# Performance work log

Hardware: AMD Instinct MI355X
Metric: run time of the kernel (lower is better)

Reference implementation:

```python
import jax, jax.numpy as jnp
import numpy as np

B, LQ, LK = 4, 256, 512
DQ, DK, DV = 512, 512, 512
H = 256
NEG = -1e6


def setup_inputs() -> dict:
    key = jax.random.key(0)
    ks = jax.random.split(key, 7)
    queries = jax.random.normal(ks[0], (B, LQ, DQ), dtype=jnp.float32)
    keys = jax.random.normal(ks[1], (B, LK, DK), dtype=jnp.float32)
    values = jax.random.normal(ks[2], (B, LK, DV), dtype=jnp.float32)
    valid_lens = jax.random.randint(ks[3], (B,), 1, LK + 1).astype(jnp.int32)
    # learned params (Linear without bias): store as (in, out) so x @ W matches torch x @ W.T
    Wq = jax.random.normal(ks[4], (DQ, H), dtype=jnp.float32) * (1.0 / np.sqrt(DQ))
    Wk = jax.random.normal(ks[5], (DK, H), dtype=jnp.float32) * (1.0 / np.sqrt(DK))
    wv = jax.random.normal(ks[6], (H,), dtype=jnp.float32) * (1.0 / np.sqrt(H))
    return {"queries": queries, "keys": keys, "values": values,
            "valid_lens": valid_lens, "Wq": Wq, "Wk": Wk, "wv": wv}


def reference(queries, keys, values, valid_lens, Wq, Wk, wv):
    q = jnp.einsum('bqd,dh->bqh', queries, Wq)          # (B,Lq,H)
    k = jnp.einsum('bkd,dh->bkh', keys, Wk)             # (B,Lk,H)
    feats = jnp.tanh(q[:, :, None, :] + k[:, None, :, :])  # (B,Lq,Lk,H)
    scores = jnp.einsum('bqkh,h->bqk', feats, wv)        # (B,Lq,Lk)
    mask = jnp.arange(LK)[None, None, :] < valid_lens[:, None, None]  # (B,1,Lk)
    attn = jax.nn.softmax(jnp.where(mask, scores, NEG), axis=-1)
    return jnp.einsum('bqk,bkv->bqv', attn, values)      # (B,Lq,Dv)
```

## Files before the change

kernel.cpp:

```cpp
#include <hip/hip_runtime.h>
#include <hip/hip_fp16.h>

#define B_   4
#define LQ_  256
#define LK_  512
#define DIN_ 512
#define H_   256
#define DV_  512

#define L2E 1.4426950408889634f

__global__ __launch_bounds__(256) void proj_partial_kernel(
    const float* __restrict__ Q, const float* __restrict__ K,
    const float* __restrict__ Wq, const float* __restrict__ Wk,
    const int* __restrict__ valid_lens,
    float* __restrict__ qpart, float* __restrict__ ekTpart) {
  __shared__ float xs[64][68];
  __shared__ float ws[64][132];

  const int blk = blockIdx.x;
  const bool isQ = blk < 128;
  int b, row0, h0, ds;
  if (isQ) {
    ds = blk & 3; h0 = ((blk >> 2) & 1) * 128;
    const int rt = blk >> 3;
    b = rt >> 2; row0 = (rt & 3) * 64;
  } else {
    const int u = blk - 128;
    ds = u & 7; h0 = ((u >> 3) & 1) * 128;
    const int rt = u >> 4;
    b = rt & 3; row0 = (rt >> 2) * 64;
    if (row0 >= valid_lens[b]) return;
  }
  const int L = isQ ? LQ_ : LK_;
  const int dspan = isQ ? 128 : 64;
  const float* __restrict__ X  = (isQ ? Q : K) + ((size_t)(b * L + row0)) * DIN_ + ds * dspan;
  const float* __restrict__ Wb = (isQ ? Wq : Wk) + (size_t)(ds * dspan) * H_ + h0;

  const int t = threadIdx.x;
  const int hthr = t & 31;
  const int rthr = t >> 5;

  float acc[8][4];
#pragma unroll
  for (int r = 0; r < 8; ++r)
#pragma unroll
    for (int c = 0; c < 4; ++c) acc[r][c] = 0.f;

  for (int dd = 0; dd < dspan; dd += 64) {
    __syncthreads();
#pragma unroll
    for (int u = 0; u < 4; ++u) {
      const int f = t + 256 * u;
      const int r = f >> 4, c4 = (f & 15) << 2;
      *(float4*)&xs[r][c4] = *(const float4*)&X[(size_t)r * DIN_ + dd + c4];
    }
#pragma unroll
    for (int u = 0; u < 8; ++u) {
      const int f = t + 256 * u;
      const int k = f >> 5, c4 = (f & 31) << 2;
      *(float4*)&ws[k][c4] = *(const float4*)&Wb[(size_t)(dd + k) * H_ + c4];
    }
    __syncthreads();

    for (int k = 0; k < 64; k += 8) {
      float4 w4[8];
#pragma unroll
      for (int k8 = 0; k8 < 8; ++k8)
        w4[k8] = *(const float4*)&ws[k + k8][4 * hthr];
#pragma unroll
      for (int rr = 0; rr < 8; ++rr) {
        const float4 xa = *(const float4*)&xs[rthr * 8 + rr][k];
        const float4 xb = *(const float4*)&xs[rthr * 8 + rr][k + 4];
        const float xv[8] = {xa.x, xa.y, xa.z, xa.w, xb.x, xb.y, xb.z, xb.w};
#pragma unroll
        for (int k8 = 0; k8 < 8; ++k8) {
          acc[rr][0] = fmaf(xv[k8], w4[k8].x, acc[rr][0]);
          acc[rr][1] = fmaf(xv[k8], w4[k8].y, acc[rr][1]);
          acc[rr][2] = fmaf(xv[k8], w4[k8].z, acc[rr][2]);
          acc[rr][3] = fmaf(xv[k8], w4[k8].w, acc[rr][3]);
        }
      }
    }
  }

  if (isQ) {
    float* dst = qpart + (size_t)ds * (B_ * LQ_ * H_);
#pragma unroll
    for (int rr = 0; rr < 8; ++rr) {
      const int row = row0 + rthr * 8 + rr;
      float4 o = {acc[rr][0], acc[rr][1], acc[rr][2], acc[rr][3]};
      *(float4*)&dst[(size_t)(b * LQ_ + row) * H_ + h0 + 4 * hthr] = o;
    }
  } else {
    float* dst = ekTpart + (size_t)ds * (B_ * H_ * LK_);
#pragma unroll
    for (int c = 0; c < 4; ++c) {
      const int h = h0 + 4 * hthr + c;
      float* p = &dst[((size_t)b * H_ + h) * LK_ + row0 + rthr * 8];
      float4 lo = {acc[0][c], acc[1][c], acc[2][c], acc[3][c]};
      float4 hi = {acc[4][c], acc[5][c], acc[6][c], acc[7][c]};
      *(float4*)p = lo;
      *(float4*)(p + 4) = hi;
    }
  }
}

__global__ __launch_bounds__(512) void combine_kernel(
    const float* __restrict__ ekTpart, const float* __restrict__ V,
    const float* __restrict__ wv,
    float* __restrict__ ek2, __half* __restrict__ Vh, float* __restrict__ wsum) {
  const int blk = blockIdx.x;
  const int t = threadIdx.x;
  if (blk < 256) {
    const int k4 = blk * 512 + t;
    const size_t KN4 = (size_t)B_ * H_ * LK_ / 4;
    const float4* src = (const float4*)ekTpart;
    float4 s = src[k4];
#pragma unroll
    for (int p = 1; p < 8; ++p) {
      const float4 v = src[p * KN4 + k4];
      s.x += v.x; s.y += v.y; s.z += v.z; s.w += v.w;
    }
    float4 o;
    o.x = exp2f(fminf(fmaxf(s.x * (2.f * L2E), -126.f), 126.f));
    o.y = exp2f(fminf(fmaxf(s.y * (2.f * L2E), -126.f), 126.f));
    o.z = exp2f(fminf(fmaxf(s.z * (2.f * L2E), -126.f), 126.f));
    o.w = exp2f(fminf(fmaxf(s.w * (2.f * L2E), -126.f), 126.f));
    ((float4*)ek2)[k4] = o;
    if (blk == 0 && t < 64) {
      float sw = wv[t] + wv[t + 64] + wv[t + 128] + wv[t + 192];
#pragma unroll
      for (int off = 32; off; off >>= 1) sw += __shfl_xor(sw, off);
      if (t == 0) *wsum = sw;
    }
  } else {
    const int q4 = (blk - 256) * 512 + t;
    const float4 v = ((const float4*)V)[q4];
    ((__half2*)Vh)[2 * q4]     = __floats2half2_rn(v.x, v.y);
    ((__half2*)Vh)[2 * q4 + 1] = __floats2half2_rn(v.z, v.w);
  }
}

__global__ __launch_bounds__(256) void scores_exp_kernel(
    const float* __restrict__ qpart, const float* __restrict__ ek2,
    const float* __restrict__ wv, const float* __restrict__ wsum,
    const int* __restrict__ valid_lens,
    float* __restrict__ e_out, float* __restrict__ sums) {
  __shared__ float eqs[2][260];
  __shared__ float wvs[256];
  __shared__ float red[4];

  const int blk = blockIdx.x;
  const int b  = blk & 3;
  const int c  = (blk >> 2) & 3;
  const int ip = blk >> 4;
  const int i0 = ip * 2;
  const int vl = valid_lens[b];
  const int j0 = c * 128;
  if (j0 >= vl) return;
  const int t = threadIdx.x;
  const int jj = t & 127, row = t >> 7;

  const size_t QN = (size_t)B_ * LQ_ * H_;
#pragma unroll
  for (int u = 0; u < 2; ++u) {
    const int idx = t + 256 * u;
    const int i = idx >> 8, h = idx & 255;
    const size_t base = (size_t)(b * LQ_ + i0 + i) * H_ + h;
    const float v = qpart[base] + qpart[QN + base] +
                    qpart[2 * QN + base] + qpart[3 * QN + base];
    eqs[i][h] = exp2f(fminf(fmaxf(v * (2.f * L2E), -126.f), 126.f));
  }
  wvs[t] = wv[t];
  __syncthreads();
  const float Wsum = *wsum;

  const int j = j0 + jj;
  float eexp = 0.f;
  if (j < vl) {
    const float* __restrict__ kb = ek2 + (size_t)b * H_ * LK_ + j;
    float a = 0.f;
    for (int h = 0; h < H_; h += 16) {
      float kv[16];
#pragma unroll
      for (int u = 0; u < 16; ++u)
        kv[u] = kb[(size_t)(h + u) * LK_];
#pragma unroll
      for (int g = 0; g < 4; ++g) {
        const float4 w4 = *(const float4*)&wvs[h + 4 * g];
        const float4 q4 = *(const float4*)&eqs[row][h + 4 * g];
        const float ww[4] = {w4.x, w4.y, w4.z, w4.w};
        const float qq[4] = {q4.x, q4.y, q4.z, q4.w};
#pragma unroll
        for (int u = 0; u < 4; ++u)
          a = fmaf(ww[u], __builtin_amdgcn_rcpf(fmaf(qq[u], kv[4 * g + u], 1.f)), a);
      }
    }
    const float score = fmaf(-2.f, a, Wsum);
    eexp = exp2f(score * L2E);
    e_out[(size_t)(b * LQ_ + i0 + row) * LK_ + j] = eexp;
  }
  float s = eexp;
#pragma unroll
  for (int off = 32; off; off >>= 1) s += __shfl_xor(s, off);
  if ((t & 63) == 0) red[t >> 6] = s;
  __syncthreads();
  if (t == 0)   sums[(size_t)(b * LQ_ + i0) * 4 + c]     = red[0] + red[1];
  if (t == 128) sums[(size_t)(b * LQ_ + i0 + 1) * 4 + c] = red[2] + red[3];
}

__global__ __launch_bounds__(512) void av_kernel(
    const float* __restrict__ e_in, const float* __restrict__ sums,
    const __half* __restrict__ Vh, const int* __restrict__ valid_lens,
    float* __restrict__ out) {
  const int blk = blockIdx.x;
  const int b  = (blk & 3) ^ ((blk >> 8) & 1);
  const int i0 = (blk >> 2) * 2;
  const int vl = valid_lens[b];
  const int t = threadIdx.x;

  const int nc = min(4, (vl + 127) >> 7);
  float tot0 = 0.f, tot1 = 0.f;
  for (int c = 0; c < nc; ++c) {
    tot0 += sums[(size_t)(b * LQ_ + i0) * 4 + c];
    tot1 += sums[(size_t)(b * LQ_ + i0 + 1) * 4 + c];
  }
  const float inv0 = __builtin_amdgcn_rcpf(tot0);
  const float inv1 = __builtin_amdgcn_rcpf(tot1);

  const float* __restrict__ e0 = e_in + (size_t)(b * LQ_ + i0) * LK_;
  const float* __restrict__ e1 = e0 + LK_;
  const __half* __restrict__ Vb = Vh + (size_t)b * LK_ * DV_ + t;

  float a0 = 0.f, a1 = 0.f;
  int j = 0;
  const int jv = vl & ~7;
  for (; j < jv; j += 8) {
    float v[8];
#pragma unroll
    for (int u = 0; u < 8; ++u)
      v[u] = __half2float(Vb[(size_t)(j + u) * DV_]);
#pragma unroll
    for (int u = 0; u < 8; ++u) {
      a0 = fmaf(e0[j + u], v[u], a0);
      a1 = fmaf(e1[j + u], v[u], a1);
    }
  }
  for (; j < vl; ++j) {
    const float v = __half2float(Vb[(size_t)j * DV_]);
    a0 = fmaf(e0[j], v, a0);
    a1 = fmaf(e1[j], v, a1);
  }
  out[(size_t)(b * LQ_ + i0) * DV_ + t]     = a0 * inv0;
  out[(size_t)(b * LQ_ + i0 + 1) * DV_ + t] = a1 * inv1;
}

extern "C" void kernel_launch(void* const* d_in, const int* in_sizes, int n_in,
                              void* d_out, int out_size, void* d_ws, size_t ws_size,
                              hipStream_t stream) {
  const float* queries    = (const float*)d_in[0];
  const float* keys       = (const float*)d_in[1];
  const float* values     = (const float*)d_in[2];
  const int*   valid_lens = (const int*)d_in[3];
  const float* Wq         = (const float*)d_in[4];
  const float* Wk         = (const float*)d_in[5];
  const float* wv         = (const float*)d_in[6];
  float* out = (float*)d_out;

  char* ws = (char*)d_ws;
  float*  qpart   = (float*)ws;
  float*  ekTpart = (float*)(ws + (size_t)( 4 << 20));
  float*  ek2     = (float*)(ws + (size_t)(20 << 20));
  float*  e_buf   = (float*)(ws + (size_t)(22 << 20));
  __half* Vh      = (__half*)(ws + (size_t)(24 << 20));
  float*  sums    = (float*)(ws + (size_t)(26 << 20));
  float*  wsum    = (float*)(ws + (size_t)(26 << 20) + 16384);

  proj_partial_kernel<<<640, 256, 0, stream>>>(
      queries, keys, Wq, Wk, valid_lens, qpart, ekTpart);
  combine_kernel<<<768, 512, 0, stream>>>(
      ekTpart, values, wv, ek2, Vh, wsum);
  scores_exp_kernel<<<2048, 256, 0, stream>>>(
      qpart, ek2, wv, wsum, valid_lens, e_buf, sums);
  av_kernel<<<512, 512, 0, stream>>>(
      e_buf, sums, Vh, valid_lens, out);
}
```

Measured before the change: 64.42 us.

## Precompute exp(2q) in combine kernel and process four query rows per block

Moves the reduction of the four q partial sums and their exponentiation out of the scores kernel and into the combine kernel, which now writes a separate eq2 buffer. The scores kernel then handles four query rows per block, two per thread, so each loaded ek2 value is reused twice and the grid halves. The AV kernel likewise computes four rows per block so each fp16 V load is reused four times, at the cost of fewer blocks (256) and lower parallelism. The batch-swizzle used for load balancing in the AV kernel is dropped.

```diff
diff --git a/kernel.cpp b/kernel.cpp
--- a/kernel.cpp
+++ b/kernel.cpp
@@ -107,13 +107,36 @@
 }
 
 __global__ __launch_bounds__(512) void combine_kernel(
-    const float* __restrict__ ekTpart, const float* __restrict__ V,
-    const float* __restrict__ wv,
-    float* __restrict__ ek2, __half* __restrict__ Vh, float* __restrict__ wsum) {
+    const float* __restrict__ qpart, const float* __restrict__ ekTpart,
+    const float* __restrict__ V, const float* __restrict__ wv,
+    float* __restrict__ eq2, float* __restrict__ ek2,
+    __half* __restrict__ Vh, float* __restrict__ wsum) {
   const int blk = blockIdx.x;
   const int t = threadIdx.x;
-  if (blk < 256) {
+  if (blk < 128) {
     const int k4 = blk * 512 + t;
+    const size_t QN4 = (size_t)B_ * LQ_ * H_ / 4;
+    const float4* src = (const float4*)qpart;
+    float4 s = src[k4];
+#pragma unroll
+    for (int p = 1; p < 4; ++p) {
+      const float4 v = src[p * QN4 + k4];
+      s.x += v.x; s.y += v.y; s.z += v.z; s.w += v.w;
+    }
+    float4 o;
+    o.x = exp2f(fminf(fmaxf(s.x * (2.f * L2E), -126.f), 126.f));
+    o.y = exp2f(fminf(fmaxf(s.y * (2.f * L2E), -126.f), 126.f));
+    o.z = exp2f(fminf(fmaxf(s.z * (2.f * L2E), -126.f), 126.f));
+    o.w = exp2f(fminf(fmaxf(s.w * (2.f * L2E), -126.f), 126.f));
+    ((float4*)eq2)[k4] = o;
+    if (blk == 0 && t < 64) {
+      float sw = wv[t] + wv[t + 64] + wv[t + 128] + wv[t + 192];
+#pragma unroll
+      for (int off = 32; off; off >>= 1) sw += __shfl_xor(sw, off);
+      if (t == 0) *wsum = sw;
+    }
+  } else if (blk < 384) {
+    const int k4 = (blk - 128) * 512 + t;
     const size_t KN4 = (size_t)B_ * H_ * LK_ / 4;
     const float4* src = (const float4*)ekTpart;
     float4 s = src[k4];
@@ -128,14 +151,8 @@
     o.z = exp2f(fminf(fmaxf(s.z * (2.f * L2E), -126.f), 126.f));
     o.w = exp2f(fminf(fmaxf(s.w * (2.f * L2E), -126.f), 126.f));
     ((float4*)ek2)[k4] = o;
-    if (blk == 0 && t < 64) {
-      float sw = wv[t] + wv[t + 64] + wv[t + 128] + wv[t + 192];
-#pragma unroll
-      for (int off = 32; off; off >>= 1) sw += __shfl_xor(sw, off);
-      if (t == 0) *wsum = sw;
-    }
   } else {
-    const int q4 = (blk - 256) * 512 + t;
+    const int q4 = (blk - 384) * 512 + t;
     const float4 v = ((const float4*)V)[q4];
     ((__half2*)Vh)[2 * q4]     = __floats2half2_rn(v.x, v.y);
     ((__half2*)Vh)[2 * q4 + 1] = __floats2half2_rn(v.z, v.w);
@@ -143,44 +160,39 @@
 }
 
 __global__ __launch_bounds__(256) void scores_exp_kernel(
-    const float* __restrict__ qpart, const float* __restrict__ ek2,
+    const float* __restrict__ eq2, const float* __restrict__ ek2,
     const float* __restrict__ wv, const float* __restrict__ wsum,
     const int* __restrict__ valid_lens,
     float* __restrict__ e_out, float* __restrict__ sums) {
-  __shared__ float eqs[2][260];
+  __shared__ float eqs[4][260];
   __shared__ float wvs[256];
-  __shared__ float red[4];
+  __shared__ float red[4][2];
 
   const int blk = blockIdx.x;
   const int b  = blk & 3;
   const int c  = (blk >> 2) & 3;
   const int ip = blk >> 4;
-  const int i0 = ip * 2;
+  const int i0 = ip * 4;
   const int vl = valid_lens[b];
   const int j0 = c * 128;
   if (j0 >= vl) return;
   const int t = threadIdx.x;
-  const int jj = t & 127, row = t >> 7;
-
-  const size_t QN = (size_t)B_ * LQ_ * H_;
-#pragma unroll
-  for (int u = 0; u < 2; ++u) {
-    const int idx = t + 256 * u;
-    const int i = idx >> 8, h = idx & 255;
-    const size_t base = (size_t)(b * LQ_ + i0 + i) * H_ + h;
-    const float v = qpart[base] + qpart[QN + base] +
-                    qpart[2 * QN + base] + qpart[3 * QN + base];
-    eqs[i][h] = exp2f(fminf(fmaxf(v * (2.f * L2E), -126.f), 126.f));
+  const int jj = t & 127, rp = t >> 7;
+
+  {
+    const int r = t >> 6, c4 = (t & 63) << 2;
+    *(float4*)&eqs[r][c4] =
+        *(const float4*)&eq2[(size_t)(b * LQ_ + i0 + r) * H_ + c4];
   }
   wvs[t] = wv[t];
   __syncthreads();
   const float Wsum = *wsum;
 
   const int j = j0 + jj;
-  float eexp = 0.f;
+  float e0 = 0.f, e1 = 0.f;
   if (j < vl) {
     const float* __restrict__ kb = ek2 + (size_t)b * H_ * LK_ + j;
-    float a = 0.f;
+    float a0 = 0.f, a1 = 0.f;
     for (int h = 0; h < H_; h += 16) {
       float kv[16];
 #pragma unroll
@@ -188,26 +200,38 @@
         kv[u] = kb[(size_t)(h + u) * LK_];
 #pragma unroll
       for (int g = 0; g < 4; ++g) {
-        const float4 w4 = *(const float4*)&wvs[h + 4 * g];
-        const float4 q4 = *(const float4*)&eqs[row][h + 4 * g];
+        const float4 w4  = *(const float4*)&wvs[h + 4 * g];
+        const float4 q0v = *(const float4*)&eqs[2 * rp][h + 4 * g];
+        const float4 q1v = *(const float4*)&eqs[2 * rp + 1][h + 4 * g];
         const float ww[4] = {w4.x, w4.y, w4.z, w4.w};
-        const float qq[4] = {q4.x, q4.y, q4.z, q4.w};
-#pragma unroll
-        for (int u = 0; u < 4; ++u)
-          a = fmaf(ww[u], __builtin_amdgcn_rcpf(fmaf(qq[u], kv[4 * g + u], 1.f)), a);
+        const float q0[4] = {q0v.x, q0v.y, q0v.z, q0v.w};
+        const float q1[4] = {q1v.x, q1v.y, q1v.z, q1v.w};
+#pragma unroll
+        for (int u = 0; u < 4; ++u) {
+          const float k2 = kv[4 * g + u];
+          a0 = fmaf(ww[u], __builtin_amdgcn_rcpf(fmaf(q0[u], k2, 1.f)), a0);
+          a1 = fmaf(ww[u], __builtin_amdgcn_rcpf(fmaf(q1[u], k2, 1.f)), a1);
+        }
       }
     }
-    const float score = fmaf(-2.f, a, Wsum);
-    eexp = exp2f(score * L2E);
-    e_out[(size_t)(b * LQ_ + i0 + row) * LK_ + j] = eexp;
-  }
-  float s = eexp;
-#pragma unroll
-  for (int off = 32; off; off >>= 1) s += __shfl_xor(s, off);
-  if ((t & 63) == 0) red[t >> 6] = s;
+    e0 = exp2f(fmaf(-2.f, a0, Wsum) * L2E);
+    e1 = exp2f(fmaf(-2.f, a1, Wsum) * L2E);
+    e_out[(size_t)(b * LQ_ + i0 + 2 * rp) * LK_ + j]     = e0;
+    e_out[(size_t)(b * LQ_ + i0 + 2 * rp + 1) * LK_ + j] = e1;
+  }
+  float s0 = e0, s1 = e1;
+#pragma unroll
+  for (int off = 32; off; off >>= 1) {
+    s0 += __shfl_xor(s0, off);
+    s1 += __shfl_xor(s1, off);
+  }
+  if ((t & 63) == 0) { red[t >> 6][0] = s0; red[t >> 6][1] = s1; }
   __syncthreads();
-  if (t == 0)   sums[(size_t)(b * LQ_ + i0) * 4 + c]     = red[0] + red[1];
-  if (t == 128) sums[(size_t)(b * LQ_ + i0 + 1) * 4 + c] = red[2] + red[3];
+  if (t < 4) {
+    const int w0 = (t >> 1) * 2, sel = t & 1;
+    const float v = red[w0][sel] + red[w0 + 1][sel];
+    sums[(size_t)(b * LQ_ + i0 + t) * 4 + c] = v;
+  }
 }
 
 __global__ __launch_bounds__(512) void av_kernel(
@@ -215,25 +239,28 @@
     const __half* __restrict__ Vh, const int* __restrict__ valid_lens,
     float* __restrict__ out) {
   const int blk = blockIdx.x;
-  const int b  = (blk & 3) ^ ((blk >> 8) & 1);
-  const int i0 = (blk >> 2) * 2;
+  const int b  = blk & 3;
+  const int i0 = (blk >> 2) * 4;
   const int vl = valid_lens[b];
   const int t = threadIdx.x;
 
   const int nc = min(4, (vl + 127) >> 7);
-  float tot0 = 0.f, tot1 = 0.f;
-  for (int c = 0; c < nc; ++c) {
-    tot0 += sums[(size_t)(b * LQ_ + i0) * 4 + c];
-    tot1 += sums[(size_t)(b * LQ_ + i0 + 1) * 4 + c];
-  }
-  const float inv0 = __builtin_amdgcn_rcpf(tot0);
-  const float inv1 = __builtin_amdgcn_rcpf(tot1);
+  float inv[4];
+#pragma unroll
+  for (int r = 0; r < 4; ++r) {
+    float tot = 0.f;
+    for (int c = 0; c < nc; ++c)
+      tot += sums[(size_t)(b * LQ_ + i0 + r) * 4 + c];
+    inv[r] = __builtin_amdgcn_rcpf(tot);
+  }
 
   const float* __restrict__ e0 = e_in + (size_t)(b * LQ_ + i0) * LK_;
   const float* __restrict__ e1 = e0 + LK_;
+  const float* __restrict__ e2 = e1 + LK_;
+  const float* __restrict__ e3 = e2 + LK_;
   const __half* __restrict__ Vb = Vh + (size_t)b * LK_ * DV_ + t;
 
-  float a0 = 0.f, a1 = 0.f;
+  float a0 = 0.f, a1 = 0.f, a2 = 0.f, a3 = 0.f;
   int j = 0;
   const int jv = vl & ~7;
   for (; j < jv; j += 8) {
@@ -245,15 +272,21 @@
     for (int u = 0; u < 8; ++u) {
       a0 = fmaf(e0[j + u], v[u], a0);
       a1 = fmaf(e1[j + u], v[u], a1);
+      a2 = fmaf(e2[j + u], v[u], a2);
+      a3 = fmaf(e3[j + u], v[u], a3);
     }
   }
   for (; j < vl; ++j) {
     const float v = __half2float(Vb[(size_t)j * DV_]);
     a0 = fmaf(e0[j], v, a0);
     a1 = fmaf(e1[j], v, a1);
-  }
-  out[(size_t)(b * LQ_ + i0) * DV_ + t]     = a0 * inv0;
-  out[(size_t)(b * LQ_ + i0 + 1) * DV_ + t] = a1 * inv1;
+    a2 = fmaf(e2[j], v, a2);
+    a3 = fmaf(e3[j], v, a3);
+  }
+  out[(size_t)(b * LQ_ + i0) * DV_ + t]     = a0 * inv[0];
+  out[(size_t)(b * LQ_ + i0 + 1) * DV_ + t] = a1 * inv[1];
+  out[(size_t)(b * LQ_ + i0 + 2) * DV_ + t] = a2 * inv[2];
+  out[(size_t)(b * LQ_ + i0 + 3) * DV_ + t] = a3 * inv[3];
 }
 
 extern "C" void kernel_launch(void* const* d_in, const int* in_sizes, int n_in,
@@ -271,18 +304,19 @@
   char* ws = (char*)d_ws;
   float*  qpart   = (float*)ws;
   float*  ekTpart = (float*)(ws + (size_t)( 4 << 20));
-  float*  ek2     = (float*)(ws + (size_t)(20 << 20));
-  float*  e_buf   = (float*)(ws + (size_t)(22 << 20));
-  __half* Vh      = (__half*)(ws + (size_t)(24 << 20));
-  float*  sums    = (float*)(ws + (size_t)(26 << 20));
-  float*  wsum    = (float*)(ws + (size_t)(26 << 20) + 16384);
+  float*  eq2     = (float*)(ws + (size_t)(20 << 20));
+  float*  ek2     = (float*)(ws + (size_t)(21 << 20));
+  float*  e_buf   = (float*)(ws + (size_t)(23 << 20));
+  __half* Vh      = (__half*)(ws + (size_t)(25 << 20));
+  float*  sums    = (float*)(ws + (size_t)(27 << 20));
+  float*  wsum    = (float*)(ws + (size_t)(27 << 20) + 16384);
 
   proj_partial_kernel<<<640, 256, 0, stream>>>(
       queries, keys, Wq, Wk, valid_lens, qpart, ekTpart);
-  combine_kernel<<<768, 512, 0, stream>>>(
-      ekTpart, values, wv, ek2, Vh, wsum);
-  scores_exp_kernel<<<2048, 256, 0, stream>>>(
-      qpart, ek2, wv, wsum, valid_lens, e_buf, sums);
-  av_kernel<<<512, 512, 0, stream>>>(
+  combine_kernel<<<896, 512, 0, stream>>>(
+      qpart, ekTpart, values, wv, eq2, ek2, Vh, wsum);
+  scores_exp_kernel<<<1024, 256, 0, stream>>>(
+      eq2, ek2, wv, wsum, valid_lens, e_buf, sums);
+  av_kernel<<<256, 512, 0, stream>>>(
       e_buf, sums, Vh, valid_lens, out);
 }
```

New measurement: 61.26 us. -4.9%, faster.

## Fuse score/exp and attention-value kernels into one per-4-row workgroup kernel

Applied to the files above, without the earlier changes.

Merges the scores_exp and av kernels into a single 1024-thread kernel in which each workgroup handles 4 query rows. Each ek2 load is reused across the 4 rows, and the H reduction is split across thread groups, with the split chosen by valid length. Exponentials stay in LDS for the AV product, which removes the global e_buf/sums round trip and one launch. The cost is only 256 large workgroups with heavy LDS use, so occupancy drops. The AV loop also always runs over all 512 keys, using zeroed weights past valid_len.

```diff
diff --git a/kernel.cpp b/kernel.cpp
--- a/kernel.cpp
+++ b/kernel.cpp
@@ -142,118 +142,173 @@
   }
 }
 
-__global__ __launch_bounds__(256) void scores_exp_kernel(
+__global__ __launch_bounds__(1024) void fused_attn_kernel(
     const float* __restrict__ qpart, const float* __restrict__ ek2,
-    const float* __restrict__ wv, const float* __restrict__ wsum,
-    const int* __restrict__ valid_lens,
-    float* __restrict__ e_out, float* __restrict__ sums) {
-  __shared__ float eqs[2][260];
+    const __half* __restrict__ Vh, const float* __restrict__ wv,
+    const float* __restrict__ wsum, const int* __restrict__ valid_lens,
+    float* __restrict__ out) {
+  __shared__ float eqs[4][260];
   __shared__ float wvs[256];
-  __shared__ float red[4];
+  __shared__ float phbuf[2 * 4 * 512];
+  __shared__ float e2s[512][4];
+  __shared__ float avp[2][512][4];
+  __shared__ float red[8][4];
+  __shared__ float tots[4];
 
   const int blk = blockIdx.x;
   const int b  = blk & 3;
-  const int c  = (blk >> 2) & 3;
-  const int ip = blk >> 4;
-  const int i0 = ip * 2;
+  const int i0 = (blk >> 2) * 4;
   const int vl = valid_lens[b];
-  const int j0 = c * 128;
-  if (j0 >= vl) return;
   const int t = threadIdx.x;
-  const int jj = t & 127, row = t >> 7;
+  const float Wsum = *wsum;
 
   const size_t QN = (size_t)B_ * LQ_ * H_;
-#pragma unroll
-  for (int u = 0; u < 2; ++u) {
-    const int idx = t + 256 * u;
-    const int i = idx >> 8, h = idx & 255;
-    const size_t base = (size_t)(b * LQ_ + i0 + i) * H_ + h;
+  {
+    const int r = t >> 8, h = t & 255;
+    const size_t base = (size_t)(b * LQ_ + i0 + r) * H_ + h;
     const float v = qpart[base] + qpart[QN + base] +
                     qpart[2 * QN + base] + qpart[3 * QN + base];
-    eqs[i][h] = exp2f(fminf(fmaxf(v * (2.f * L2E), -126.f), 126.f));
-  }
-  wvs[t] = wv[t];
+    eqs[r][h] = exp2f(fminf(fmaxf(v * (2.f * L2E), -126.f), 126.f));
+    if (r == 0) wvs[h] = wv[h];
+  }
   __syncthreads();
-  const float Wsum = *wsum;
-
-  const int j = j0 + jj;
-  float eexp = 0.f;
-  if (j < vl) {
-    const float* __restrict__ kb = ek2 + (size_t)b * H_ * LK_ + j;
-    float a = 0.f;
-    for (int h = 0; h < H_; h += 16) {
-      float kv[16];
-#pragma unroll
-      for (int u = 0; u < 16; ++u)
-        kv[u] = kb[(size_t)(h + u) * LK_];
-#pragma unroll
-      for (int g = 0; g < 4; ++g) {
-        const float4 w4 = *(const float4*)&wvs[h + 4 * g];
-        const float4 q4 = *(const float4*)&eqs[row][h + 4 * g];
-        const float ww[4] = {w4.x, w4.y, w4.z, w4.w};
-        const float qq[4] = {q4.x, q4.y, q4.z, q4.w};
-#pragma unroll
-        for (int u = 0; u < 4; ++u)
-          a = fmaf(ww[u], __builtin_amdgcn_rcpf(fmaf(qq[u], kv[4 * g + u], 1.f)), a);
-      }
-    }
-    const float score = fmaf(-2.f, a, Wsum);
-    eexp = exp2f(score * L2E);
-    e_out[(size_t)(b * LQ_ + i0 + row) * LK_ + j] = eexp;
-  }
-  float s = eexp;
-#pragma unroll
-  for (int off = 32; off; off >>= 1) s += __shfl_xor(s, off);
-  if ((t & 63) == 0) red[t >> 6] = s;
+
+#define PHA(hh, r, j) phbuf[(((hh) << 2) + (r)) * 512 + (j)]
+#define PHB(hq, r, j) phbuf[(((hq) << 2) + (r)) * 256 + (j)]
+  if (vl > 256) {
+    const int j = t & 511, hh = t >> 9;
+    if (j < vl) {
+      const float* __restrict__ kb = ek2 + (size_t)b * H_ * LK_ + j;
+      const int hb = hh * 128;
+      float a[4] = {0.f, 0.f, 0.f, 0.f};
+      for (int h2 = 0; h2 < 128; h2 += 16) {
+        const int h = hb + h2;
+        float kv[16];
+#pragma unroll
+        for (int u = 0; u < 16; ++u)
+          kv[u] = kb[(size_t)(h + u) * LK_];
+#pragma unroll
+        for (int g = 0; g < 4; ++g) {
+          const float4 w4 = *(const float4*)&wvs[h + 4 * g];
+          const float ww[4] = {w4.x, w4.y, w4.z, w4.w};
+#pragma unroll
+          for (int r = 0; r < 4; ++r) {
+            const float4 q4 = *(const float4*)&eqs[r][h + 4 * g];
+            const float qq[4] = {q4.x, q4.y, q4.z, q4.w};
+#pragma unroll
+            for (int u = 0; u < 4; ++u)
+              a[r] = fmaf(ww[u],
+                  __builtin_amdgcn_rcpf(fmaf(qq[u], kv[4 * g + u], 1.f)), a[r]);
+          }
+        }
+      }
+#pragma unroll
+      for (int r = 0; r < 4; ++r) PHA(hh, r, j) = a[r];
+    }
+  } else {
+    const int j = t & 255, hq = t >> 8;
+    if (j < vl) {
+      const float* __restrict__ kb = ek2 + (size_t)b * H_ * LK_ + j;
+      const int hb = hq * 64;
+      float a[4] = {0.f, 0.f, 0.f, 0.f};
+      for (int h2 = 0; h2 < 64; h2 += 16) {
+        const int h = hb + h2;
+        float kv[16];
+#pragma unroll
+        for (int u = 0; u < 16; ++u)
+          kv[u] = kb[(size_t)(h + u) * LK_];
+#pragma unroll
+        for (int g = 0; g < 4; ++g) {
+          const float4 w4 = *(const float4*)&wvs[h + 4 * g];
+          const float ww[4] = {w4.x, w4.y, w4.z, w4.w};
+#pragma unroll
+          for (int r = 0; r < 4; ++r) {
+            const float4 q4 = *(const float4*)&eqs[r][h + 4 * g];
+            const float qq[4] = {q4.x, q4.y, q4.z, q4.w};
+#pragma unroll
+            for (int u = 0; u < 4; ++u)
+              a[r] = fmaf(ww[u],
+                  __builtin_amdgcn_rcpf(fmaf(qq[u], kv[4 * g + u], 1.f)), a[r]);
+          }
+        }
+      }
+#pragma unroll
+      for (int r = 0; r < 4; ++r) PHB(hq, r, j) = a[r];
+    }
+  }
   __syncthreads();
-  if (t == 0)   sums[(size_t)(b * LQ_ + i0) * 4 + c]     = red[0] + red[1];
-  if (t == 128) sums[(size_t)(b * LQ_ + i0 + 1) * 4 + c] = red[2] + red[3];
-}
-
-__global__ __launch_bounds__(512) void av_kernel(
-    const float* __restrict__ e_in, const float* __restrict__ sums,
-    const __half* __restrict__ Vh, const int* __restrict__ valid_lens,
-    float* __restrict__ out) {
-  const int blk = blockIdx.x;
-  const int b  = (blk & 3) ^ ((blk >> 8) & 1);
-  const int i0 = (blk >> 2) * 2;
-  const int vl = valid_lens[b];
-  const int t = threadIdx.x;
-
-  const int nc = min(4, (vl + 127) >> 7);
-  float tot0 = 0.f, tot1 = 0.f;
-  for (int c = 0; c < nc; ++c) {
-    tot0 += sums[(size_t)(b * LQ_ + i0) * 4 + c];
-    tot1 += sums[(size_t)(b * LQ_ + i0 + 1) * 4 + c];
-  }
-  const float inv0 = __builtin_amdgcn_rcpf(tot0);
-  const float inv1 = __builtin_amdgcn_rcpf(tot1);
-
-  const float* __restrict__ e0 = e_in + (size_t)(b * LQ_ + i0) * LK_;
-  const float* __restrict__ e1 = e0 + LK_;
-  const __half* __restrict__ Vb = Vh + (size_t)b * LK_ * DV_ + t;
-
-  float a0 = 0.f, a1 = 0.f;
-  int j = 0;
-  const int jv = vl & ~7;
-  for (; j < jv; j += 8) {
-    float v[8];
-#pragma unroll
-    for (int u = 0; u < 8; ++u)
-      v[u] = __half2float(Vb[(size_t)(j + u) * DV_]);
-#pragma unroll
-    for (int u = 0; u < 8; ++u) {
-      a0 = fmaf(e0[j + u], v[u], a0);
-      a1 = fmaf(e1[j + u], v[u], a1);
-    }
-  }
-  for (; j < vl; ++j) {
-    const float v = __half2float(Vb[(size_t)j * DV_]);
-    a0 = fmaf(e0[j], v, a0);
-    a1 = fmaf(e1[j], v, a1);
-  }
-  out[(size_t)(b * LQ_ + i0) * DV_ + t]     = a0 * inv0;
-  out[(size_t)(b * LQ_ + i0 + 1) * DV_ + t] = a1 * inv1;
+
+  if (t < 512) {
+    const int j = t;
+    float er[4] = {0.f, 0.f, 0.f, 0.f};
+    if (j < vl) {
+      if (vl > 256) {
+#pragma unroll
+        for (int r = 0; r < 4; ++r) {
+          const float a = PHA(0, r, j) + PHA(1, r, j);
+          er[r] = exp2f(fmaf(-2.f, a, Wsum) * L2E);
+        }
+      } else {
+#pragma unroll
+        for (int r = 0; r < 4; ++r) {
+          const float a = PHB(0, r, j) + PHB(1, r, j) + PHB(2, r, j) + PHB(3, r, j);
+          er[r] = exp2f(fmaf(-2.f, a, Wsum) * L2E);
+        }
+      }
+    }
+    *(float4*)&e2s[j][0] = *(float4*)er;
+    float s0 = er[0], s1 = er[1], s2 = er[2], s3 = er[3];
+#pragma unroll
+    for (int off = 32; off; off >>= 1) {
+      s0 += __shfl_xor(s0, off); s1 += __shfl_xor(s1, off);
+      s2 += __shfl_xor(s2, off); s3 += __shfl_xor(s3, off);
+    }
+    if ((t & 63) == 0) {
+      const int w = t >> 6;
+      red[w][0] = s0; red[w][1] = s1; red[w][2] = s2; red[w][3] = s3;
+    }
+  }
+  __syncthreads();
+  if (t < 4) {
+    float s = 0.f;
+#pragma unroll
+    for (int w = 0; w < 8; ++w) s += red[w][t];
+    tots[t] = s;
+  }
+
+  {
+    const int col = t & 511, jh = t >> 9;
+    const __half* __restrict__ Vb = Vh + (size_t)b * LK_ * DV_ + col;
+    float a0 = 0.f, a1 = 0.f, a2 = 0.f, a3 = 0.f;
+    const int jbase = jh * 256;
+    for (int j = jbase; j < jbase + 256; j += 8) {
+      float v[8];
+#pragma unroll
+      for (int u = 0; u < 8; ++u)
+        v[u] = __half2float(Vb[(size_t)(j + u) * DV_]);
+#pragma unroll
+      for (int u = 0; u < 8; ++u) {
+        const float4 ee = *(const float4*)&e2s[j + u][0];
+        a0 = fmaf(ee.x, v[u], a0); a1 = fmaf(ee.y, v[u], a1);
+        a2 = fmaf(ee.z, v[u], a2); a3 = fmaf(ee.w, v[u], a3);
+      }
+    }
+    float o[4] = {a0, a1, a2, a3};
+    *(float4*)&avp[jh][col][0] = *(float4*)o;
+  }
+  __syncthreads();
+  if (t < 512) {
+    const float4 x0 = *(const float4*)&avp[0][t][0];
+    const float4 x1 = *(const float4*)&avp[1][t][0];
+    const float i0r = __builtin_amdgcn_rcpf(tots[0]);
+    const float i1r = __builtin_amdgcn_rcpf(tots[1]);
+    const float i2r = __builtin_amdgcn_rcpf(tots[2]);
+    const float i3r = __builtin_amdgcn_rcpf(tots[3]);
+    out[(size_t)(b * LQ_ + i0) * DV_ + t]     = (x0.x + x1.x) * i0r;
+    out[(size_t)(b * LQ_ + i0 + 1) * DV_ + t] = (x0.y + x1.y) * i1r;
+    out[(size_t)(b * LQ_ + i0 + 2) * DV_ + t] = (x0.z + x1.z) * i2r;
+    out[(size_t)(b * LQ_ + i0 + 3) * DV_ + t] = (x0.w + x1.w) * i3r;
+  }
 }
 
 extern "C" void kernel_launch(void* const* d_in, const int* in_sizes, int n_in,
@@ -272,17 +327,13 @@
   float*  qpart   = (float*)ws;
   float*  ekTpart = (float*)(ws + (size_t)( 4 << 20));
   float*  ek2     = (float*)(ws + (size_t)(20 << 20));
-  float*  e_buf   = (float*)(ws + (size_t)(22 << 20));
-  __half* Vh      = (__half*)(ws + (size_t)(24 << 20));
-  float*  sums    = (float*)(ws + (size_t)(26 << 20));
-  float*  wsum    = (float*)(ws + (size_t)(26 << 20) + 16384);
+  __half* Vh      = (__half*)(ws + (size_t)(22 << 20));
+  float*  wsum    = (float*)(ws + (size_t)(24 << 20));
 
   proj_partial_kernel<<<640, 256, 0, stream>>>(
       queries, keys, Wq, Wk, valid_lens, qpart, ekTpart);
   combine_kernel<<<768, 512, 0, stream>>>(
       ekTpart, values, wv, ek2, Vh, wsum);
-  scores_exp_kernel<<<2048, 256, 0, stream>>>(
-      qpart, ek2, wv, wsum, valid_lens, e_buf, sums);
-  av_kernel<<<512, 512, 0, stream>>>(
-      e_buf, sums, Vh, valid_lens, out);
+  fused_attn_kernel<<<256, 1024, 0, stream>>>(
+      qpart, ek2, Vh, wv, wsum, valid_lens, out);
 }
```

New measurement: 55.51 us. -13.8%, faster.
